# Performance work log

Hardware: AMD Instinct MI355X
Metric: run time of the kernel (lower is better)

The kernel has to match this reference:

```python
import jax, jax.numpy as jnp
import numpy as np

HIDDEN = 4096
N_HEADS = 32
N_KV_HEADS = 8
HEAD_DIM = 128
N_GROUPS = N_HEADS // N_KV_HEADS
ROPE_THETA = 10000.0
QMAX = 127.0
B, S = 1, 2048


def setup_inputs() -> dict:
    key = jax.random.key(0)
    ks = jax.random.split(key, 5)
    hidden_states = jax.random.normal(ks[0], (B, S, HIDDEN), dtype=jnp.float32)
    # additive causal mask (Llama style: 0 on/below diagonal, large negative above)
    tril = jnp.tril(jnp.ones((S, S), dtype=bool))
    attention_mask = jnp.where(tril, 0.0, -1e9).astype(jnp.float32)[None, None]
    position_ids = jnp.arange(S, dtype=jnp.int64 if jax.config.jax_enable_x64 else jnp.int32)[None].astype(jnp.int32)
    sc = 1.0 / np.sqrt(HIDDEN)
    wq = jax.random.normal(ks[1], (HIDDEN, N_HEADS * HEAD_DIM), dtype=jnp.float32) * sc
    wk = jax.random.normal(ks[2], (HIDDEN, N_KV_HEADS * HEAD_DIM), dtype=jnp.float32) * sc
    wv = jax.random.normal(ks[3], (HIDDEN, N_KV_HEADS * HEAD_DIM), dtype=jnp.float32) * sc
    wo = jax.random.normal(ks[4], (N_HEADS * HEAD_DIM, HIDDEN), dtype=jnp.float32) * sc
    return {"hidden_states": hidden_states, "attention_mask": attention_mask,
            "position_ids": position_ids, "wq": wq, "wk": wk, "wv": wv, "wo": wo}


def _rope_cos_sin(position_ids):
    # [B, S, HEAD_DIM]
    inv_freq = 1.0 / (ROPE_THETA ** (jnp.arange(0, HEAD_DIM, 2, dtype=jnp.float32) / HEAD_DIM))
    freqs = position_ids.astype(jnp.float32)[..., None] * inv_freq  # [B,S,HEAD_DIM//2]
    emb = jnp.concatenate([freqs, freqs], axis=-1)
    return jnp.cos(emb), jnp.sin(emb)


def _rotate_half(x):
    x1, x2 = jnp.split(x, 2, axis=-1)
    return jnp.concatenate([-x2, x1], axis=-1)


def _fake_quant(x):
    scale = jnp.max(jnp.abs(x)) / QMAX  # global absmax
    return jnp.round(x / scale) * scale


def reference(hidden_states, attention_mask, position_ids, wq, wk, wv, wo):
    bsz, q_len, _ = hidden_states.shape
    q = (hidden_states @ wq).reshape(bsz, q_len, N_HEADS, HEAD_DIM).transpose(0, 2, 1, 3)
    k = (hidden_states @ wk).reshape(bsz, q_len, N_KV_HEADS, HEAD_DIM).transpose(0, 2, 1, 3)
    v = (hidden_states @ wv).reshape(bsz, q_len, N_KV_HEADS, HEAD_DIM).transpose(0, 2, 1, 3)

    cos, sin = _rope_cos_sin(position_ids)  # [B,S,D]
    cos, sin = cos[:, None], sin[:, None]   # broadcast over heads
    q = q * cos + _rotate_half(q) * sin
    k = k * cos + _rotate_half(k) * sin

    # repeat_kv: [B, Hkv, S, D] -> [B, H, S, D]
    k = jnp.repeat(k, N_GROUPS, axis=1)
    v = jnp.repeat(v, N_GROUPS, axis=1)

    # fake quant: global absmax round-trip on Q, K, V
    q = _fake_quant(q)
    k = _fake_quant(k)
    v = _fake_quant(v)

    scores = jnp.einsum('bhqd,bhkd->bhqk', q, k) / np.sqrt(HEAD_DIM)
    scores = scores + attention_mask
    probs = jax.nn.softmax(scores.astype(jnp.float32), axis=-1).astype(q.dtype)
    attn = jnp.einsum('bhqk,bhkd->bhqd', probs, v)
    attn = attn.transpose(0, 2, 1, 3).reshape(bsz, q_len, N_HEADS * HEAD_DIM)
    return attn @ wo
```

## Files before the change

kernel.cpp:

```cpp
#include <hip/hip_runtime.h>
#include <math.h>

#define S_LEN 2048
#define HID 4096
#define NH 32
#define NKV 8
#define HD 128
#define NQKV 6144

typedef __bf16 bf16x8 __attribute__((ext_vector_type(8)));
typedef float f32x4 __attribute__((ext_vector_type(4)));
typedef short short8v __attribute__((ext_vector_type(8)));

__device__ inline short f2bf(float f) {
  union { float f; unsigned u; } a; a.f = f;
  unsigned r = a.u + 0x7fffu + ((a.u >> 16) & 1u);
  return (short)(r >> 16);
}

__device__ inline void glds16(const void* g, void* l) {
  __builtin_amdgcn_global_load_lds((const __attribute__((address_space(1))) void*)g,
                                   (__attribute__((address_space(3))) void*)l, 16, 0, 0);
}

template <int CTRL>
__device__ inline float dpp_max_step(float x) {
  int y = __builtin_amdgcn_update_dpp(0, __float_as_int(x), CTRL, 0xf, 0xf, false);
  return fmaxf(x, __int_as_float(y));
}

__global__ __launch_bounds__(256) void cast_h(const float* __restrict__ X,
                                              short* __restrict__ Y, int n4) {
  int i = blockIdx.x * 256 + threadIdx.x;
  if (i >= n4) return;
  float4 v = ((const float4*)X)[i];
  short4 o;
  o.x = f2bf(v.x); o.y = f2bf(v.y); o.z = f2bf(v.z); o.w = f2bf(v.w);
  ((short4*)Y)[i] = o;
}

__global__ __launch_bounds__(256) void cast_wt(const float* __restrict__ W,
                                               short* __restrict__ Wt, int Ncols) {
  __shared__ float t[32][33];
  int n0 = blockIdx.x * 32, k0 = blockIdx.y * 32;
  int tx = threadIdx.x, ty = threadIdx.y;
  for (int j = 0; j < 4; j++)
    t[ty + 8 * j][tx] = W[(size_t)(k0 + ty + 8 * j) * Ncols + n0 + tx];
  __syncthreads();
  for (int j = 0; j < 4; j++)
    Wt[(size_t)(n0 + ty + 8 * j) * 4096 + k0 + tx] = f2bf(t[tx][ty + 8 * j]);
}

__global__ void rope_table(const int* __restrict__ pos_ids, float* __restrict__ tc,
                           float* __restrict__ ts) {
  int p = blockIdx.x, i = threadIdx.x;
  float pos = (float)pos_ids[p];
  float inv = powf(10000.0f, -((float)(2 * i)) * (1.0f / 128.0f));
  float a = pos * inv;
  tc[p * 64 + i] = cosf(a);
  ts[p * 64 + i] = sinf(a);
}

__global__ __launch_bounds__(256) void rope_absmax(float* __restrict__ C,
                                                   const float* __restrict__ tc,
                                                   const float* __restrict__ ts,
                                                   unsigned* __restrict__ scal) {
  __shared__ float lc[64], lsn[64];
  __shared__ float red[3][4];
  const int p = blockIdx.x, t = threadIdx.x;
  if (t < 64) { lc[t] = tc[p * 64 + t]; lsn[t] = ts[p * 64 + t]; }
  __syncthreads();
  float* row = C + (size_t)p * NQKV;
  float mq = 0.f, mk = 0.f, mv = 0.f;
#pragma unroll
  for (int j = 0; j < 8; j++) {
    int idx = t + 256 * j;
    int i = idx & 63, col = (idx >> 6) * 128 + i;
    float c = lc[i], s = lsn[i];
    float x1 = row[col], x2 = row[col + 64];
    float y1 = x1 * c - x2 * s, y2 = x2 * c + x1 * s;
    row[col] = y1; row[col + 64] = y2;
    mq = fmaxf(mq, fmaxf(fabsf(y1), fabsf(y2)));
  }
#pragma unroll
  for (int j = 0; j < 2; j++) {
    int idx = t + 256 * j;
    int i = idx & 63, col = 4096 + (idx >> 6) * 128 + i;
    float c = lc[i], s = lsn[i];
    float x1 = row[col], x2 = row[col + 64];
    float y1 = x1 * c - x2 * s, y2 = x2 * c + x1 * s;
    row[col] = y1; row[col + 64] = y2;
    mk = fmaxf(mk, fmaxf(fabsf(y1), fabsf(y2)));
  }
#pragma unroll
  for (int j = 0; j < 4; j++) {
    float v = row[5120 + t + 256 * j];
    mv = fmaxf(mv, fabsf(v));
  }
  for (int off = 32; off; off >>= 1) {
    mq = fmaxf(mq, __shfl_xor(mq, off, 64));
    mk = fmaxf(mk, __shfl_xor(mk, off, 64));
    mv = fmaxf(mv, __shfl_xor(mv, off, 64));
  }
  const int wave = t >> 6;
  if ((t & 63) == 0) { red[0][wave] = mq; red[1][wave] = mk; red[2][wave] = mv; }
  __syncthreads();
  if (t < 3) {
    float m = fmaxf(fmaxf(red[t][0], red[t][1]), fmaxf(red[t][2], red[t][3]));
    atomicMax(scal + t, __float_as_uint(m));
  }
}

__global__ __launch_bounds__(256) void quant_q(const float* __restrict__ C,
                                               const unsigned* __restrict__ scal,
                                               short* __restrict__ Qi) {
  int idx = blockIdx.x * 256 + threadIdx.x;
  float scale = __uint_as_float(scal[0]) * (1.0f / 127.0f);
  int p = idx >> 12, c = idx & 4095;
  Qi[idx] = f2bf(rintf(C[(size_t)p * NQKV + c] / scale));
}

__global__ __launch_bounds__(256) void quant_k(const float* __restrict__ C,
                                               const unsigned* __restrict__ scal,
                                               short* __restrict__ Ki) {
  int idx = blockIdx.x * 256 + threadIdx.x;
  float scale = __uint_as_float(scal[1]) * (1.0f / 127.0f);
  int h = idx >> 18, p = (idx >> 7) & 2047, d = idx & 127;
  Ki[idx] = f2bf(rintf(C[(size_t)p * NQKV + 4096 + h * 128 + d] / scale));
}

__global__ __launch_bounds__(256) void quant_vt(const float* __restrict__ C,
                                                const unsigned* __restrict__ scal,
                                                short* __restrict__ Vt) {
  __shared__ float t[64][65];
  int h = blockIdx.x, pt = blockIdx.y, dt = blockIdx.z;
  float scale = __uint_as_float(scal[2]) * (1.0f / 127.0f);
  int tid = threadIdx.x;
  for (int j = 0; j < 16; j++) {
    int q = tid + 256 * j;
    int pl = q >> 6, dl = q & 63;
    t[dl][pl] = C[(size_t)(pt * 64 + pl) * NQKV + 5120 + h * 128 + dt * 64 + dl];
  }
  __syncthreads();
  for (int j = 0; j < 16; j++) {
    int q = tid + 256 * j;
    int dl = q >> 6, pl = q & 63;
    Vt[(size_t)(h * 128 + dt * 64 + dl) * 2048 + pt * 64 + pl] =
        f2bf(rintf(t[dl][pl] / scale));
  }
}

__global__ __launch_bounds__(256, 2) void gemm_bt(const short* __restrict__ A, int lda,
                                                  const short* __restrict__ B,
                                                  float* __restrict__ C, int ldc, int K) {
  __shared__ alignas(16) short As[2][4096];
  __shared__ alignas(16) short Bs[2][4096];
  const int tid = threadIdx.x;
  const int wave = tid >> 6, lane = tid & 63;
  const int quad = lane >> 4, l15 = lane & 15;
  const int m0 = blockIdx.y * 128, n0 = blockIdx.x * 128;
  const int wm = (wave >> 1) * 64, wn = (wave & 1) * 64;
  f32x4 acc[4][4] = {};
  const int sr = wave * 16 + (lane >> 2);
  const int sg = (lane & 3) * 8;
  const short* Ag0 = A + (size_t)(m0 + sr) * lda + sg;
  const short* Ag1 = A + (size_t)(m0 + 64 + sr) * lda + sg;
  const short* Bg0 = B + (size_t)(n0 + sr) * K + sg;
  const short* Bg1 = B + (size_t)(n0 + 64 + sr) * K + sg;
  auto stage = [&](int kk, int b) {
    glds16(Ag0 + kk, &As[b][wave * 512]);
    glds16(Ag1 + kk, &As[b][2048 + wave * 512]);
    glds16(Bg0 + kk, &Bs[b][wave * 512]);
    glds16(Bg1 + kk, &Bs[b][2048 + wave * 512]);
  };
  stage(0, 0);
  int b = 0;
  for (int k0 = 0; k0 < K; k0 += 32) {
    __syncthreads();
    const int nk = (k0 + 32 < K) ? k0 + 32 : k0;
    stage(nk, b ^ 1);
    bf16x8 af[4], bfr[4];
#pragma unroll
    for (int t = 0; t < 4; t++) {
      af[t] = *(const bf16x8*)&As[b][(wm + t * 16 + l15) * 32 + quad * 8];
      bfr[t] = *(const bf16x8*)&Bs[b][(wn + t * 16 + l15) * 32 + quad * 8];
    }
#pragma unroll
    for (int tm = 0; tm < 4; tm++)
#pragma unroll
      for (int tn = 0; tn < 4; tn++)
        acc[tm][tn] =
            __builtin_amdgcn_mfma_f32_16x16x32_bf16(af[tm], bfr[tn], acc[tm][tn], 0, 0, 0);
    b ^= 1;
  }
#pragma unroll
  for (int tm = 0; tm < 4; tm++)
#pragma unroll
    for (int tn = 0; tn < 4; tn++) {
      const int row = m0 + wm + tm * 16 + quad * 4;
      const int col = n0 + wn + tn * 16 + l15;
#pragma unroll
      for (int r = 0; r < 4; r++) C[(size_t)(row + r) * ldc + col] = acc[tm][tn][r];
    }
}

__global__ __launch_bounds__(512, 2) void gemm_bt8(const short* __restrict__ A, int lda,
                                                   const short* __restrict__ B, int ldb,
                                                   float* __restrict__ C, int ldc, int K) {
  __shared__ alignas(16) short As[2][16384];
  __shared__ alignas(16) short Bs[2][16384];
  const int tid = threadIdx.x;
  const int wave = tid >> 6, lane = tid & 63;
  const int quad = lane >> 4, l15 = lane & 15;
  const int wm = wave >> 2, wn = wave & 3;
  const int m0 = blockIdx.y * 256, n0 = blockIdx.x * 256;

  const int rsub = lane >> 3;
  const int csw = (lane & 7) ^ rsub;
  size_t asrc[4], bsrc[4];
#pragma unroll
  for (int s = 0; s < 4; s++) {
    int row = s * 64 + wave * 8 + rsub;
    asrc[s] = (size_t)(m0 + row) * lda + csw * 8;
    bsrc[s] = (size_t)(n0 + row) * ldb + csw * 8;
  }
  const int nt = K >> 6;

  auto stA = [&](int t2) {
    const int kk = (t2 < nt ? t2 : nt - 1) << 6;
#pragma unroll
    for (int s = 0; s < 4; s++)
      glds16(A + asrc[s] + kk, &As[t2 & 1][(s * 64 + wave * 8) * 64]);
  };
  auto stB = [&](int t2) {
    const int kk = (t2 < nt ? t2 : nt - 1) << 6;
#pragma unroll
    for (int s = 0; s < 4; s++)
      glds16(B + bsrc[s] + kk, &Bs[t2 & 1][(s * 64 + wave * 8) * 64]);
  };

  int swq[2];
#pragma unroll
  for (int kc = 0; kc < 2; kc++)
    swq[kc] = l15 * 64 + (((kc * 4 + quad) ^ (l15 & 7)) * 8);

  f32x4 acc[8][4] = {};

  stB(0); stA(0);
  stB(1);
  asm volatile("s_waitcnt vmcnt(4)" ::: "memory");
  __builtin_amdgcn_s_barrier();

  for (int t = 0; t < nt; t++) {
    const short* Ab = As[t & 1];
    const short* Bb = Bs[t & 1];
    stA(t + 1);
    bf16x8 bfr[4][2];
#pragma unroll
    for (int n = 0; n < 4; n++) {
      bfr[n][0] = *(const bf16x8*)&Bb[(wn * 64 + n * 16) * 64 + swq[0]];
      bfr[n][1] = *(const bf16x8*)&Bb[(wn * 64 + n * 16) * 64 + swq[1]];
    }
    asm volatile("s_waitcnt lgkmcnt(0)" ::: "memory");
    __builtin_amdgcn_sched_barrier(0);
    __builtin_amdgcn_s_barrier();
    stB(t + 2);
    __builtin_amdgcn_s_setprio(1);
#pragma unroll
    for (int m = 0; m < 8; m++) {
      bf16x8 a0 = *(const bf16x8*)&Ab[(wm * 128 + m * 16) * 64 + swq[0]];
      bf16x8 a1 = *(const bf16x8*)&Ab[(wm * 128 + m * 16) * 64 + swq[1]];
#pragma unroll
      for (int n = 0; n < 4; n++) {
        acc[m][n] = __builtin_amdgcn_mfma_f32_16x16x32_bf16(a0, bfr[n][0], acc[m][n], 0, 0, 0);
        acc[m][n] = __builtin_amdgcn_mfma_f32_16x16x32_bf16(a1, bfr[n][1], acc[m][n], 0, 0, 0);
      }
    }
    __builtin_amdgcn_s_setprio(0);
    asm volatile("s_waitcnt vmcnt(4)" ::: "memory");
    __builtin_amdgcn_s_barrier();
    __builtin_amdgcn_sched_barrier(0);
  }
#pragma unroll
  for (int m = 0; m < 8; m++)
#pragma unroll
    for (int n = 0; n < 4; n++) {
      const int row = m0 + wm * 128 + m * 16 + quad * 4;
      const int col = n0 + wn * 64 + n * 16 + l15;
#pragma unroll
      for (int r = 0; r < 4; r++) C[(size_t)(row + r) * ldc + col] = acc[m][n][r];
    }
}

__global__ __launch_bounds__(256, 2) void attn_fused(const short* __restrict__ Qi,
                                                     const short* __restrict__ Ki,
                                                     const short* __restrict__ Vt,
                                                     const unsigned* __restrict__ scal,
                                                     short* __restrict__ Oa) {
  __shared__ alignas(16) short Ks[2][64 * 128];
  __shared__ alignas(16) short Vs[2][128 * 64];
  __shared__ alignas(16) short Ps[4][16 * 72];
  const int tid = threadIdx.x;
  const int wave = tid >> 6, lane = tid & 63;
  const int quad = lane >> 4, l15 = lane & 15;
  const int swz = l15 & 7;
  const int h = blockIdx.x & 31, pq = blockIdx.x >> 5;
  const int kvh = h >> 2;
  const float qs = __uint_as_float(scal[0]) * (1.0f / 127.0f);
  const float ksc = __uint_as_float(scal[1]) * (1.0f / 127.0f);
  const float vsc = __uint_as_float(scal[2]) * (1.0f / 127.0f);
  const float sscale = qs * ksc * 0.08838834764831845f * 1.4426950408889634f;
  const short* Kg = Ki + (size_t)kvh * S_LEN * HD;
  const short* Vg = Vt + (size_t)kvh * HD * S_LEN;

  union { short8v s; bf16x8 b; } uone;
  uone.s = short8v{0x3F80, 0x3F80, 0x3F80, 0x3F80, 0x3F80, 0x3F80, 0x3F80, 0x3F80};
  const bf16x8 vone = uone.b;

  int koff[4], voff[4];
#pragma unroll
  for (int j = 0; j < 4; j++) {
    int slot = j * 256 + tid;
    int r = slot >> 4, seg = slot & 15;
    koff[j] = r * 128 + ((seg ^ (r & 7)) * 8);
    int vr = slot >> 3, vseg = slot & 7;
    voff[j] = vr * 2048 + ((vseg ^ (vr & 7)) * 8);
  }
  auto stage = [&](int k0, int b) {
#pragma unroll
    for (int j = 0; j < 4; j++)
      glds16(Kg + (size_t)k0 * HD + koff[j], &Ks[b][(j * 256 + wave * 64) * 8]);
#pragma unroll
    for (int j = 0; j < 4; j++)
      glds16(Vg + (size_t)k0 + voff[j], &Vs[b][(j * 256 + wave * 64) * 8]);
  };

  stage(0, 0);
  int buf = 0;
  for (int ph = 0; ph < 2; ph++) {
    const int qt = ph ? 31 - pq : pq;
    const int rw = qt * 64 + wave * 16;
    bf16x8 aq[4];
#pragma unroll
    for (int kc = 0; kc < 4; kc++)
      aq[kc] = *(const bf16x8*)(Qi + (size_t)(rw + l15) * 4096 + h * 128 + kc * 32 +
                                quad * 8);
    f32x4 o[9] = {};
    float m_[4] = {-INFINITY, -INFINITY, -INFINITY, -INFINITY};
    const int nkt = qt + 1;
    for (int kt = 0; kt < nkt; kt++) {
      const int k0 = kt * 64;
      __syncthreads();
      const int nx = (kt + 1 < nkt) ? k0 + 64 : 0;
      stage(nx, buf ^ 1);

      const short* Kb = Ks[buf];
      const short* Vb = Vs[buf];
      f32x4 sf[4];
      __builtin_amdgcn_s_setprio(1);
#pragma unroll
      for (int tn = 0; tn < 4; tn++) {
        f32x4 s = {0.f, 0.f, 0.f, 0.f};
#pragma unroll
        for (int kc = 0; kc < 4; kc++) {
          bf16x8 bk = *(const bf16x8*)&Kb[(tn * 16 + l15) * 128 + ((kc * 4 + quad) ^ swz) * 8];
          s = __builtin_amdgcn_mfma_f32_16x16x32_bf16(aq[kc], bk, s, 0, 0, 0);
        }
        sf[tn] = s;
      }
      __builtin_amdgcn_s_setprio(0);

      const bool diag = (kt == qt);
#pragma unroll
      for (int r = 0; r < 4; r++) {
        const int grow = rw + quad * 4 + r;
        float mx = -3.0e38f;
        if (diag) {
#pragma unroll
          for (int tn = 0; tn < 4; tn++) {
            float v = sf[tn][r] * sscale;
            if (k0 + tn * 16 + l15 > grow) v = -3.0e38f;
            sf[tn][r] = v;
            mx = fmaxf(mx, v);
          }
        } else {
#pragma unroll
          for (int tn = 0; tn < 4; tn++) {
            float v = sf[tn][r] * sscale;
            sf[tn][r] = v;
            mx = fmaxf(mx, v);
          }
        }
        mx = dpp_max_step<0x121>(mx);
        mx = dpp_max_step<0x122>(mx);
        mx = dpp_max_step<0x124>(mx);
        mx = dpp_max_step<0x128>(mx);
        const float mo = m_[r];
        const float mn = fmaxf(mo, mx);
        m_[r] = mn;
        const float alpha = __builtin_amdgcn_exp2f(mo - mn);
#pragma unroll
        for (int tn = 0; tn < 4; tn++) {
          float p = __builtin_amdgcn_exp2f(sf[tn][r] - mn);
          Ps[wave][(quad * 4 + r) * 72 + tn * 16 + l15] =
              (short)((__float_as_uint(p) + 0x8000u) >> 16);
        }
        if (__ballot(alpha != 1.0f)) {
#pragma unroll
          for (int t = 0; t < 9; t++) o[t][r] *= alpha;
        }
      }
      __builtin_amdgcn_s_setprio(1);
#pragma unroll
      for (int kk = 0; kk < 2; kk++) {
        bf16x8 ap = *(const bf16x8*)&Ps[wave][l15 * 72 + kk * 32 + quad * 8];
#pragma unroll
        for (int tn = 0; tn < 8; tn++) {
          bf16x8 bv = *(const bf16x8*)&Vb[(tn * 16 + l15) * 64 + ((kk * 4 + quad) ^ swz) * 8];
          o[tn] = __builtin_amdgcn_mfma_f32_16x16x32_bf16(ap, bv, o[tn], 0, 0, 0);
        }
        o[8] = __builtin_amdgcn_mfma_f32_16x16x32_bf16(ap, vone, o[8], 0, 0, 0);
      }
      __builtin_amdgcn_s_setprio(0);
      buf ^= 1;
    }
#pragma unroll
    for (int r = 0; r < 4; r++) {
      const int grow = rw + quad * 4 + r;
      const float sc = vsc / o[8][r];
#pragma unroll
      for (int tn = 0; tn < 8; tn++)
        Oa[(size_t)grow * 4096 + h * 128 + tn * 16 + l15] = f2bf(o[tn][r] * sc);
    }
  }
}

extern "C" void kernel_launch(void* const* d_in, const int* in_sizes, int n_in,
                              void* d_out, int out_size, void* d_ws, size_t ws_size,
                              hipStream_t stream) {
  (void)in_sizes; (void)n_in; (void)out_size; (void)ws_size;
  const float* H  = (const float*)d_in[0];
  const int*   pos = (const int*)d_in[2];
  const float* wq = (const float*)d_in[3];
  const float* wk = (const float*)d_in[4];
  const float* wv = (const float*)d_in[5];
  const float* wo = (const float*)d_in[6];
  char* ws = (char*)d_ws;
  short* Hb   = (short*)(ws + 0);
  short* Wt   = (short*)(ws + 16777216);
  short* Wot  = (short*)(ws + 67108864);
  float* C    = (float*)(ws + 100663296);
  short* Qi   = (short*)(ws + 150994944);
  short* Ki   = (short*)(ws + 167772160);
  short* Vt   = (short*)(ws + 171966464);
  short* Oa   = (short*)(ws + 176160768);
  float* tc   = (float*)(ws + 192937984);
  float* tsn  = (float*)(ws + 193462272);
  unsigned* scal = (unsigned*)(ws + 193986560);

  hipLaunchKernelGGL(cast_h, dim3(8192), dim3(256), 0, stream, H, Hb, 2097152);
  hipLaunchKernelGGL(cast_wt, dim3(128, 128), dim3(32, 8), 0, stream, wq, Wt, 4096);
  hipLaunchKernelGGL(cast_wt, dim3(32, 128), dim3(32, 8), 0, stream, wk,
                     Wt + (size_t)4096 * 4096, 1024);
  hipLaunchKernelGGL(cast_wt, dim3(32, 128), dim3(32, 8), 0, stream, wv,
                     Wt + (size_t)5120 * 4096, 1024);
  hipLaunchKernelGGL(cast_wt, dim3(128, 128), dim3(32, 8), 0, stream, wo, Wot, 4096);
  hipLaunchKernelGGL(rope_table, dim3(2048), dim3(64), 0, stream, pos, tc, tsn);
  hipMemsetAsync(scal, 0, 16, stream);
  hipLaunchKernelGGL(gemm_bt8, dim3(24, 8), dim3(512), 0, stream, Hb, 4096, Wt, 4096, C,
                     6144, 4096);
  hipLaunchKernelGGL(rope_absmax, dim3(2048), dim3(256), 0, stream, C, tc, tsn, scal);
  hipLaunchKernelGGL(quant_q, dim3(32768), dim3(256), 0, stream, C, scal, Qi);
  hipLaunchKernelGGL(quant_k, dim3(8192), dim3(256), 0, stream, C, scal, Ki);
  hipLaunchKernelGGL(quant_vt, dim3(8, 32, 2), dim3(256), 0, stream, C, scal, Vt);
  hipLaunchKernelGGL(attn_fused, dim3(512), dim3(256), 0, stream, Qi, Ki, Vt, scal, Oa);
  hipLaunchKernelGGL(gemm_bt, dim3(32, 16), dim3(256), 0, stream, Oa, 4096, Wot,
                     (float*)d_out, 4096, 4096);
}
```

Before: 596.7 us.

## Merge prep, cast and quant kernels; use 128-tile GEMM for QKV projection

Fuses the input cast, RoPE table build and scale reset into one prep kernel, the four weight casts into one launch, and the three quantization kernels into one. This removes several launches and the memset. It also replaces the 256x256 gemm_bt8 QKV projection with the smaller 128x128 gemm_bt kernel, and drops the s_setprio hints in attention. The GEMM swap trades tile reuse for more blocks, and cast_wt_all launches many blocks that exit early for the K/V slices.

```diff
diff --git a/kernel.cpp b/kernel.cpp
--- a/kernel.cpp
+++ b/kernel.cpp
@@ -29,36 +29,54 @@
   return fmaxf(x, __int_as_float(y));
 }
 
-__global__ __launch_bounds__(256) void cast_h(const float* __restrict__ X,
-                                              short* __restrict__ Y, int n4) {
-  int i = blockIdx.x * 256 + threadIdx.x;
-  if (i >= n4) return;
-  float4 v = ((const float4*)X)[i];
-  short4 o;
-  o.x = f2bf(v.x); o.y = f2bf(v.y); o.z = f2bf(v.z); o.w = f2bf(v.w);
-  ((short4*)Y)[i] = o;
-}
-
-__global__ __launch_bounds__(256) void cast_wt(const float* __restrict__ W,
-                                               short* __restrict__ Wt, int Ncols) {
+__global__ __launch_bounds__(256) void prep(const float* __restrict__ X,
+                                            short* __restrict__ Y,
+                                            const int* __restrict__ pos_ids,
+                                            float* __restrict__ tc,
+                                            float* __restrict__ ts,
+                                            unsigned* __restrict__ scal) {
+  const int b = blockIdx.x, t = threadIdx.x;
+  if (b < 8192) {
+    int i = b * 256 + t;
+    float4 v = ((const float4*)X)[i];
+    short4 o;
+    o.x = f2bf(v.x); o.y = f2bf(v.y); o.z = f2bf(v.z); o.w = f2bf(v.w);
+    ((short4*)Y)[i] = o;
+  } else {
+    const int bb = b - 8192;
+    const int p = bb * 4 + (t >> 6);
+    const int i = t & 63;
+    float pos = (float)pos_ids[p];
+    float inv = powf(10000.0f, -((float)(2 * i)) * (1.0f / 128.0f));
+    float a = pos * inv;
+    tc[p * 64 + i] = cosf(a);
+    ts[p * 64 + i] = sinf(a);
+    if (bb == 0 && t < 4) scal[t] = 0u;
+  }
+}
+
+__global__ __launch_bounds__(256) void cast_wt_all(const float* __restrict__ wq,
+                                                   const float* __restrict__ wk,
+                                                   const float* __restrict__ wv,
+                                                   const float* __restrict__ wo,
+                                                   short* __restrict__ Wt,
+                                                   short* __restrict__ Wot) {
   __shared__ float t[32][33];
-  int n0 = blockIdx.x * 32, k0 = blockIdx.y * 32;
-  int tx = threadIdx.x, ty = threadIdx.y;
+  const int z = blockIdx.z;
+  const float* W; short* dst; int Ncols;
+  if (z == 0)      { W = wq; dst = Wt;                            Ncols = 4096; }
+  else if (z == 1) { W = wk; dst = Wt + (size_t)4096 * 4096;      Ncols = 1024; }
+  else if (z == 2) { W = wv; dst = Wt + (size_t)5120 * 4096;      Ncols = 1024; }
+  else             { W = wo; dst = Wot;                           Ncols = 4096; }
+  const int n0 = blockIdx.x * 32;
+  if (n0 >= Ncols) return;
+  const int k0 = blockIdx.y * 32;
+  const int tx = threadIdx.x, ty = threadIdx.y;
   for (int j = 0; j < 4; j++)
     t[ty + 8 * j][tx] = W[(size_t)(k0 + ty + 8 * j) * Ncols + n0 + tx];
   __syncthreads();
   for (int j = 0; j < 4; j++)
-    Wt[(size_t)(n0 + ty + 8 * j) * 4096 + k0 + tx] = f2bf(t[tx][ty + 8 * j]);
-}
-
-__global__ void rope_table(const int* __restrict__ pos_ids, float* __restrict__ tc,
-                           float* __restrict__ ts) {
-  int p = blockIdx.x, i = threadIdx.x;
-  float pos = (float)pos_ids[p];
-  float inv = powf(10000.0f, -((float)(2 * i)) * (1.0f / 128.0f));
-  float a = pos * inv;
-  tc[p * 64 + i] = cosf(a);
-  ts[p * 64 + i] = sinf(a);
+    dst[(size_t)(n0 + ty + 8 * j) * 4096 + k0 + tx] = f2bf(t[tx][ty + 8 * j]);
 }
 
 __global__ __launch_bounds__(256) void rope_absmax(float* __restrict__ C,
@@ -111,42 +129,39 @@
   }
 }
 
-__global__ __launch_bounds__(256) void quant_q(const float* __restrict__ C,
-                                               const unsigned* __restrict__ scal,
-                                               short* __restrict__ Qi) {
-  int idx = blockIdx.x * 256 + threadIdx.x;
-  float scale = __uint_as_float(scal[0]) * (1.0f / 127.0f);
-  int p = idx >> 12, c = idx & 4095;
-  Qi[idx] = f2bf(rintf(C[(size_t)p * NQKV + c] / scale));
-}
-
-__global__ __launch_bounds__(256) void quant_k(const float* __restrict__ C,
-                                               const unsigned* __restrict__ scal,
-                                               short* __restrict__ Ki) {
-  int idx = blockIdx.x * 256 + threadIdx.x;
-  float scale = __uint_as_float(scal[1]) * (1.0f / 127.0f);
-  int h = idx >> 18, p = (idx >> 7) & 2047, d = idx & 127;
-  Ki[idx] = f2bf(rintf(C[(size_t)p * NQKV + 4096 + h * 128 + d] / scale));
-}
-
-__global__ __launch_bounds__(256) void quant_vt(const float* __restrict__ C,
-                                                const unsigned* __restrict__ scal,
-                                                short* __restrict__ Vt) {
-  __shared__ float t[64][65];
-  int h = blockIdx.x, pt = blockIdx.y, dt = blockIdx.z;
-  float scale = __uint_as_float(scal[2]) * (1.0f / 127.0f);
-  int tid = threadIdx.x;
-  for (int j = 0; j < 16; j++) {
-    int q = tid + 256 * j;
-    int pl = q >> 6, dl = q & 63;
-    t[dl][pl] = C[(size_t)(pt * 64 + pl) * NQKV + 5120 + h * 128 + dt * 64 + dl];
-  }
-  __syncthreads();
-  for (int j = 0; j < 16; j++) {
-    int q = tid + 256 * j;
-    int dl = q >> 6, pl = q & 63;
-    Vt[(size_t)(h * 128 + dt * 64 + dl) * 2048 + pt * 64 + pl] =
-        f2bf(rintf(t[dl][pl] / scale));
+__global__ __launch_bounds__(256) void quant_all(const float* __restrict__ C,
+                                                 const unsigned* __restrict__ scal,
+                                                 short* __restrict__ Qi,
+                                                 short* __restrict__ Ki,
+                                                 short* __restrict__ Vt) {
+  __shared__ float tile[64][65];
+  const int b = blockIdx.x, t = threadIdx.x;
+  if (b < 32768) {
+    int idx = b * 256 + t;
+    float scale = __uint_as_float(scal[0]) * (1.0f / 127.0f);
+    int p = idx >> 12, c = idx & 4095;
+    Qi[idx] = f2bf(rintf(C[(size_t)p * NQKV + c] / scale));
+  } else if (b < 40960) {
+    int idx = (b - 32768) * 256 + t;
+    float scale = __uint_as_float(scal[1]) * (1.0f / 127.0f);
+    int h = idx >> 18, p = (idx >> 7) & 2047, d = idx & 127;
+    Ki[idx] = f2bf(rintf(C[(size_t)p * NQKV + 4096 + h * 128 + d] / scale));
+  } else {
+    const int bb = b - 40960;
+    const int h = bb >> 6, pt = (bb >> 1) & 31, dt = bb & 1;
+    float scale = __uint_as_float(scal[2]) * (1.0f / 127.0f);
+    for (int j = 0; j < 16; j++) {
+      int q = t + 256 * j;
+      int pl = q >> 6, dl = q & 63;
+      tile[dl][pl] = C[(size_t)(pt * 64 + pl) * NQKV + 5120 + h * 128 + dt * 64 + dl];
+    }
+    __syncthreads();
+    for (int j = 0; j < 16; j++) {
+      int q = t + 256 * j;
+      int dl = q >> 6, pl = q & 63;
+      Vt[(size_t)(h * 128 + dt * 64 + dl) * 2048 + pt * 64 + pl] =
+          f2bf(rintf(tile[dl][pl] / scale));
+    }
   }
 }
 
@@ -204,94 +219,6 @@
     }
 }
 
-__global__ __launch_bounds__(512, 2) void gemm_bt8(const short* __restrict__ A, int lda,
-                                                   const short* __restrict__ B, int ldb,
-                                                   float* __restrict__ C, int ldc, int K) {
-  __shared__ alignas(16) short As[2][16384];
-  __shared__ alignas(16) short Bs[2][16384];
-  const int tid = threadIdx.x;
-  const int wave = tid >> 6, lane = tid & 63;
-  const int quad = lane >> 4, l15 = lane & 15;
-  const int wm = wave >> 2, wn = wave & 3;
-  const int m0 = blockIdx.y * 256, n0 = blockIdx.x * 256;
-
-  const int rsub = lane >> 3;
-  const int csw = (lane & 7) ^ rsub;
-  size_t asrc[4], bsrc[4];
-#pragma unroll
-  for (int s = 0; s < 4; s++) {
-    int row = s * 64 + wave * 8 + rsub;
-    asrc[s] = (size_t)(m0 + row) * lda + csw * 8;
-    bsrc[s] = (size_t)(n0 + row) * ldb + csw * 8;
-  }
-  const int nt = K >> 6;
-
-  auto stA = [&](int t2) {
-    const int kk = (t2 < nt ? t2 : nt - 1) << 6;
-#pragma unroll
-    for (int s = 0; s < 4; s++)
-      glds16(A + asrc[s] + kk, &As[t2 & 1][(s * 64 + wave * 8) * 64]);
-  };
-  auto stB = [&](int t2) {
-    const int kk = (t2 < nt ? t2 : nt - 1) << 6;
-#pragma unroll
-    for (int s = 0; s < 4; s++)
-      glds16(B + bsrc[s] + kk, &Bs[t2 & 1][(s * 64 + wave * 8) * 64]);
-  };
-
-  int swq[2];
-#pragma unroll
-  for (int kc = 0; kc < 2; kc++)
-    swq[kc] = l15 * 64 + (((kc * 4 + quad) ^ (l15 & 7)) * 8);
-
-  f32x4 acc[8][4] = {};
-
-  stB(0); stA(0);
-  stB(1);
-  asm volatile("s_waitcnt vmcnt(4)" ::: "memory");
-  __builtin_amdgcn_s_barrier();
-
-  for (int t = 0; t < nt; t++) {
-    const short* Ab = As[t & 1];
-    const short* Bb = Bs[t & 1];
-    stA(t + 1);
-    bf16x8 bfr[4][2];
-#pragma unroll
-    for (int n = 0; n < 4; n++) {
-      bfr[n][0] = *(const bf16x8*)&Bb[(wn * 64 + n * 16) * 64 + swq[0]];
-      bfr[n][1] = *(const bf16x8*)&Bb[(wn * 64 + n * 16) * 64 + swq[1]];
-    }
-    asm volatile("s_waitcnt lgkmcnt(0)" ::: "memory");
-    __builtin_amdgcn_sched_barrier(0);
-    __builtin_amdgcn_s_barrier();
-    stB(t + 2);
-    __builtin_amdgcn_s_setprio(1);
-#pragma unroll
-    for (int m = 0; m < 8; m++) {
-      bf16x8 a0 = *(const bf16x8*)&Ab[(wm * 128 + m * 16) * 64 + swq[0]];
-      bf16x8 a1 = *(const bf16x8*)&Ab[(wm * 128 + m * 16) * 64 + swq[1]];
-#pragma unroll
-      for (int n = 0; n < 4; n++) {
-        acc[m][n] = __builtin_amdgcn_mfma_f32_16x16x32_bf16(a0, bfr[n][0], acc[m][n], 0, 0, 0);
-        acc[m][n] = __builtin_amdgcn_mfma_f32_16x16x32_bf16(a1, bfr[n][1], acc[m][n], 0, 0, 0);
-      }
-    }
-    __builtin_amdgcn_s_setprio(0);
-    asm volatile("s_waitcnt vmcnt(4)" ::: "memory");
-    __builtin_amdgcn_s_barrier();
-    __builtin_amdgcn_sched_barrier(0);
-  }
-#pragma unroll
-  for (int m = 0; m < 8; m++)
-#pragma unroll
-    for (int n = 0; n < 4; n++) {
-      const int row = m0 + wm * 128 + m * 16 + quad * 4;
-      const int col = n0 + wn * 64 + n * 16 + l15;
-#pragma unroll
-      for (int r = 0; r < 4; r++) C[(size_t)(row + r) * ldc + col] = acc[m][n][r];
-    }
-}
-
 __global__ __launch_bounds__(256, 2) void attn_fused(const short* __restrict__ Qi,
                                                      const short* __restrict__ Ki,
                                                      const short* __restrict__ Vt,
@@ -357,7 +284,6 @@
       const short* Kb = Ks[buf];
       const short* Vb = Vs[buf];
       f32x4 sf[4];
-      __builtin_amdgcn_s_setprio(1);
 #pragma unroll
       for (int tn = 0; tn < 4; tn++) {
         f32x4 s = {0.f, 0.f, 0.f, 0.f};
@@ -368,7 +294,6 @@
         }
         sf[tn] = s;
       }
-      __builtin_amdgcn_s_setprio(0);
 
       const bool diag = (kt == qt);
 #pragma unroll
@@ -410,7 +335,6 @@
           for (int t = 0; t < 9; t++) o[t][r] *= alpha;
         }
       }
-      __builtin_amdgcn_s_setprio(1);
 #pragma unroll
       for (int kk = 0; kk < 2; kk++) {
         bf16x8 ap = *(const bf16x8*)&Ps[wave][l15 * 72 + kk * 32 + quad * 8];
@@ -421,7 +345,6 @@
         }
         o[8] = __builtin_amdgcn_mfma_f32_16x16x32_bf16(ap, vone, o[8], 0, 0, 0);
       }
-      __builtin_amdgcn_s_setprio(0);
       buf ^= 1;
     }
 #pragma unroll
@@ -458,21 +381,13 @@
   float* tsn  = (float*)(ws + 193462272);
   unsigned* scal = (unsigned*)(ws + 193986560);
 
-  hipLaunchKernelGGL(cast_h, dim3(8192), dim3(256), 0, stream, H, Hb, 2097152);
-  hipLaunchKernelGGL(cast_wt, dim3(128, 128), dim3(32, 8), 0, stream, wq, Wt, 4096);
-  hipLaunchKernelGGL(cast_wt, dim3(32, 128), dim3(32, 8), 0, stream, wk,
-                     Wt + (size_t)4096 * 4096, 1024);
-  hipLaunchKernelGGL(cast_wt, dim3(32, 128), dim3(32, 8), 0, stream, wv,
-                     Wt + (size_t)5120 * 4096, 1024);
-  hipLaunchKernelGGL(cast_wt, dim3(128, 128), dim3(32, 8), 0, stream, wo, Wot, 4096);
-  hipLaunchKernelGGL(rope_table, dim3(2048), dim3(64), 0, stream, pos, tc, tsn);
-  hipMemsetAsync(scal, 0, 16, stream);
-  hipLaunchKernelGGL(gemm_bt8, dim3(24, 8), dim3(512), 0, stream, Hb, 4096, Wt, 4096, C,
-                     6144, 4096);
+  hipLaunchKernelGGL(prep, dim3(8704), dim3(256), 0, stream, H, Hb, pos, tc, tsn, scal);
+  hipLaunchKernelGGL(cast_wt_all, dim3(128, 128, 4), dim3(32, 8), 0, stream, wq, wk, wv,
+                     wo, Wt, Wot);
+  hipLaunchKernelGGL(gemm_bt, dim3(48, 16), dim3(256), 0, stream, Hb, 4096, Wt, C, 6144,
+                     4096);
   hipLaunchKernelGGL(rope_absmax, dim3(2048), dim3(256), 0, stream, C, tc, tsn, scal);
-  hipLaunchKernelGGL(quant_q, dim3(32768), dim3(256), 0, stream, C, scal, Qi);
-  hipLaunchKernelGGL(quant_k, dim3(8192), dim3(256), 0, stream, C, scal, Ki);
-  hipLaunchKernelGGL(quant_vt, dim3(8, 32, 2), dim3(256), 0, stream, C, scal, Vt);
+  hipLaunchKernelGGL(quant_all, dim3(41472), dim3(256), 0, stream, C, scal, Qi, Ki, Vt);
   hipLaunchKernelGGL(attn_fused, dim3(512), dim3(256), 0, stream, Qi, Ki, Vt, scal, Oa);
   hipLaunchKernelGGL(gemm_bt, dim3(32, 16), dim3(256), 0, stream, Oa, 4096, Wot,
                      (float*)d_out, 4096, 4096);
```

Result: faster. 553.5 us, median of 2 (-7.2%).
